# Performance work log

Hardware: AMD Instinct MI355X
Metric: run time of the kernel (lower is better)

The kernel has to match this reference:

```python
import jax, jax.numpy as jnp
import numpy as np

B_, N, C, H = 2048, 49, 384, 12
WH, WW = 7, 7
HEAD_DIM = C // H
SCALE = HEAD_DIM ** -0.5
TABLE = (2 * WH - 1) * (2 * WW - 1)  # 169


def _relative_position_index():
    coords = np.stack(np.meshgrid(np.arange(WH), np.arange(WW), indexing='ij'))  # [2,Wh,Ww]
    flat = coords.reshape(2, -1)  # [2,N]
    rel = flat[:, :, None] - flat[:, None, :]  # [2,N,N]
    rel = rel.transpose(1, 2, 0).astype(np.int32)  # [N,N,2]
    rel[:, :, 0] += WH - 1
    rel[:, :, 1] += WW - 1
    rel[:, :, 0] *= 2 * WW - 1
    return rel.sum(-1)  # [N,N] int32 in [0,169)


def setup_inputs() -> dict:
    key = jax.random.key(0)
    ks = jax.random.split(key, 8)
    return {
        'x': jax.random.normal(ks[0], (B_, N, C), jnp.float32),
        'mask': jax.random.normal(ks[1], (B_, 1, N, N), jnp.float32),
        'stagein': jax.random.uniform(ks[2], (B_, N, C), jnp.float32),
        'rel_bias_table': jax.random.normal(ks[3], (TABLE, H), jnp.float32) * 0.02,
        'rel_pos_index': jnp.asarray(_relative_position_index()),
        'qkv_w': jax.random.normal(ks[4], (3 * C, C), jnp.float32) * 0.02,
        'qkv_b': jax.random.normal(ks[5], (3 * C,), jnp.float32) * 0.02,
        'proj_w': jax.random.normal(ks[6], (C, C), jnp.float32) * 0.02,
        'proj_b': jax.random.normal(ks[7], (C,), jnp.float32) * 0.02,
    }


def reference(x, mask, stagein, rel_bias_table, rel_pos_index, qkv_w, qkv_b, proj_w, proj_b):
    x = x * stagein  # stagein is not None branch
    qkv = x @ qkv_w.T + qkv_b  # [B_, N, 3C]
    qkv = qkv.reshape(B_, N, 3, H, HEAD_DIM).transpose(2, 0, 3, 1, 4)  # [3,B_,H,N,hd]
    q, k, v = qkv[0], qkv[1], qkv[2]
    q = q * SCALE
    attn = jnp.einsum('bhnd,bhmd->bhnm', q, k)  # [B_,H,N,N]
    # relative position bias gather: [N*N] -> [N,N,H] -> [1,H,N,N]
    bias = rel_bias_table[rel_pos_index.reshape(-1)].reshape(N, N, H)
    bias = bias.transpose(2, 0, 1)[None]
    attn = jax.nn.softmax(attn + bias + mask, axis=-1)
    out = jnp.einsum('bhnm,bhmd->bhnd', attn, v)  # [B_,H,N,hd]
    out = out.transpose(0, 2, 1, 3).reshape(B_, N, C)
    return out @ proj_w.T + proj_b
```

## Files before the change

### kernel.cpp

```cpp
#include <hip/hip_runtime.h>
#include <hip/hip_bf16.h>
#include <stdint.h>

#define NWIN 2048
#define NTOK 49
#define CDIM 384
#define NHEAD 12
#define HD 32
#define C3 1152
#define NN2 2401
#define MROWS 100352

typedef __bf16 bf16x8 __attribute__((ext_vector_type(8)));
typedef float f32x4 __attribute__((ext_vector_type(4)));
typedef uint32_t u32x4 __attribute__((ext_vector_type(4)));
typedef unsigned int u32;

static __device__ __forceinline__ unsigned short f2bf(float f) {
  uint32_t u = __builtin_bit_cast(uint32_t, f);
  u += 0x7fffu + ((u >> 16) & 1u);
  return (unsigned short)(u >> 16);
}

static __device__ __forceinline__ u32 pk2(float a, float b) {
  return (u32)f2bf(a) | ((u32)f2bf(b) << 16);
}

static __device__ __forceinline__ void gload_lds16(const void* g, void* l) {
  __builtin_amdgcn_global_load_lds((const __attribute__((address_space(1))) void*)g,
                                   (__attribute__((address_space(3))) void*)l,
                                   16, 0, 0);
}

static __device__ __forceinline__ bf16x8 zero8() {
  u32x4 z = {0u, 0u, 0u, 0u};
  return __builtin_bit_cast(bf16x8, z);
}

__global__ void prep_kernel(const float* __restrict__ qkv_w, const float* __restrict__ proj_w,
                            const float* __restrict__ table, const int* __restrict__ idx,
                            unsigned short* __restrict__ wq, unsigned short* __restrict__ wp,
                            float* __restrict__ biasT) {
  const int NW1 = C3 * CDIM;
  const int NW2 = CDIM * CDIM;
  const int NB = NHEAD * NN2;
  int i = blockIdx.x * blockDim.x + threadIdx.x;
  int stride = gridDim.x * blockDim.x;
  for (int t = i; t < NW1 + NW2 + NB; t += stride) {
    if (t < NW1) {
      wq[t] = f2bf(qkv_w[t]);
    } else if (t < NW1 + NW2) {
      int j = t - NW1;
      wp[j] = f2bf(proj_w[j]);
    } else {
      int j = t - NW1 - NW2;
      int h = j / NN2;
      int nm = j - h * NN2;
      int m = nm / 49, n = nm - m * 49;
      biasT[j] = table[idx[n * 49 + m] * NHEAD + h];
    }
  }
}

__global__ void mul_kernel(const float4* __restrict__ x, const float4* __restrict__ s,
                           u32x4* __restrict__ A, int n8) {
  int i0 = blockIdx.x * blockDim.x + threadIdx.x;
  int stride = gridDim.x * blockDim.x;
  for (int t = i0; t < n8; t += stride) {
    float4 a0 = x[2 * t], a1 = x[2 * t + 1];
    float4 b0 = s[2 * t], b1 = s[2 * t + 1];
    u32x4 o;
    o[0] = pk2(a0.x * b0.x, a0.y * b0.y);
    o[1] = pk2(a0.z * b0.z, a0.w * b0.w);
    o[2] = pk2(a1.x * b1.x, a1.y * b1.y);
    o[3] = pk2(a1.z * b1.z, a1.w * b1.w);
    A[t] = o;
  }
}

__launch_bounds__(512, 2)
__global__ void qkv_gemm(const unsigned short* __restrict__ A,
                         const unsigned short* __restrict__ Bw,
                         const float* __restrict__ qkvb,
                         unsigned short* __restrict__ qo,
                         unsigned short* __restrict__ ko,
                         unsigned short* __restrict__ vo) {
  __shared__ unsigned short As[128 * 64];
  __shared__ unsigned short Bs[128 * 64];
  const int tid = threadIdx.x;
  const int w = tid >> 6, l = tid & 63;
  const int l15 = l & 15, lhi = l >> 4;
  const int wgid = (blockIdx.x & 7) * 882 + (blockIdx.x >> 3);
  const int mt = wgid / 9, nt = wgid - mt * 9;
  const int wr = w >> 2, wc = w & 3;
  const int srow = tid >> 3;
  const int scb = (tid & 7) ^ (srow & 7);
  const unsigned short* Ag = A + (size_t)(mt * 128 + srow) * CDIM + scb * 8;
  const unsigned short* Bg = Bw + (size_t)(nt * 128 + srow) * CDIM + scb * 8;
  unsigned short* Asl = As + srow * 64 + (tid & 7) * 8;
  unsigned short* Bsl = Bs + srow * 64 + (tid & 7) * 8;
  const f32x4 z4 = {0.f, 0.f, 0.f, 0.f};
  f32x4 acc[4][2];
#pragma unroll
  for (int m = 0; m < 4; ++m)
#pragma unroll
    for (int n = 0; n < 2; ++n) acc[m][n] = z4;
  const int xr = l15 & 7;
  for (int kt = 0; kt < 6; ++kt) {
    const unsigned short* ag = Ag + kt * 64;
    const unsigned short* bg = Bg + kt * 64;
    gload_lds16(ag, Asl);
    gload_lds16(ag + 64 * CDIM, Asl + 4096);
    gload_lds16(bg, Bsl);
    gload_lds16(bg + 64 * CDIM, Bsl + 4096);
    __syncthreads();
#pragma unroll
    for (int kk = 0; kk < 2; ++kk) {
      const int sl = ((kk << 2) | lhi) ^ xr;
      bf16x8 af[4], bfr[2];
#pragma unroll
      for (int m = 0; m < 4; ++m)
        af[m] = *(const bf16x8*)(As + (wr * 64 + m * 16 + l15) * 64 + sl * 8);
#pragma unroll
      for (int n = 0; n < 2; ++n)
        bfr[n] = *(const bf16x8*)(Bs + (wc * 32 + n * 16 + l15) * 64 + sl * 8);
#pragma unroll
      for (int m = 0; m < 4; ++m)
#pragma unroll
        for (int n = 0; n < 2; ++n)
          acc[m][n] = __builtin_amdgcn_mfma_f32_16x16x32_bf16(af[m], bfr[n], acc[m][n], 0, 0, 0);
    }
    __syncthreads();
  }
  const float SCALE_F = 0.17677669529663687f;
  const int six = nt * 4 + wc;
  const int which = six / 12;
  const int cbase = (six - which * 12) * 32;
  unsigned short* outw = (which == 0) ? qo : ((which == 1) ? ko : vo);
  const float* bptr = qkvb + which * CDIM;
  float bv2[2];
#pragma unroll
  for (int n = 0; n < 2; ++n) bv2[n] = bptr[cbase + n * 16 + l15];
#pragma unroll
  for (int m = 0; m < 4; ++m) {
    const int r0 = mt * 128 + wr * 64 + m * 16 + lhi * 4;
#pragma unroll
    for (int j = 0; j < 4; ++j) {
      unsigned short* orow = outw + (size_t)(r0 + j) * CDIM;
#pragma unroll
      for (int n = 0; n < 2; ++n) {
        float val = acc[m][n][j] + bv2[n];
        if (which == 0) val *= SCALE_F;
        orow[cbase + n * 16 + l15] = f2bf(val);
      }
    }
  }
}

__launch_bounds__(768, 2)
__global__ void attn_kernel(const unsigned short* __restrict__ q,
                            const unsigned short* __restrict__ kmat,
                            const unsigned short* __restrict__ vmat,
                            const float* __restrict__ mask,
                            const float* __restrict__ biasT,
                            unsigned short* __restrict__ attnout) {
  __shared__ unsigned short vT_lds[12][32 * 72];
  __shared__ float maskLds[49 * 50];
  const int tid = threadIdx.x;
  const int w = tid >> 6, l = tid & 63;
  const int l15 = l & 15, lhi = l >> 4;
  const int b = (blockIdx.x & 7) * 256 + (blockIdx.x >> 3);
  unsigned short* Vw = &vT_lds[w][0];
  const f32x4 z4 = {0.f, 0.f, 0.f, 0.f};
  const int h = w;
  const size_t rowbase = (size_t)b * NTOK * CDIM + h * HD;
  const unsigned short* qb = q + rowbase;
  const unsigned short* kb = kmat + rowbase;
  const unsigned short* vb = vmat + rowbase;
  {
    const float* mb = mask + (size_t)b * NN2;
    for (int i = tid; i < NN2; i += 768) {
      const int n = i / 49, m = i - n * 49;
      maskLds[m * 50 + n] = mb[i];
    }
  }
  {
    const int n = l;
    unsigned short tmp[32];
    if (n < 49) {
      *(u32x4*)(&tmp[0])  = *(const u32x4*)(vb + (size_t)n * CDIM);
      *(u32x4*)(&tmp[8])  = *(const u32x4*)(vb + (size_t)n * CDIM + 8);
      *(u32x4*)(&tmp[16]) = *(const u32x4*)(vb + (size_t)n * CDIM + 16);
      *(u32x4*)(&tmp[24]) = *(const u32x4*)(vb + (size_t)n * CDIM + 24);
    } else {
#pragma unroll
      for (int d2 = 0; d2 < 32; ++d2) tmp[d2] = 0;
    }
#pragma unroll
    for (int d2 = 0; d2 < 32; ++d2) Vw[d2 * 72 + n] = tmp[d2];
  }
  bf16x8 aq[4], bk[4];
#pragma unroll
  for (int t = 0; t < 4; ++t) {
    const int row = t * 16 + l15;
    if (row < 49) {
      aq[t] = *(const bf16x8*)(qb + (size_t)row * CDIM + lhi * 8);
      bk[t] = *(const bf16x8*)(kb + (size_t)row * CDIM + lhi * 8);
    } else {
      aq[t] = zero8();
      bk[t] = zero8();
    }
  }
  __syncthreads();
  const float* biash = biasT + h * NN2;
  u32 P4[4][4][2];
#pragma unroll
  for (int nt = 0; nt < 4; ++nt) {
    f32x4 s4[4];
#pragma unroll
    for (int mt = 0; mt < 4; ++mt)
      s4[mt] = __builtin_amdgcn_mfma_f32_16x16x32_bf16(bk[mt], aq[nt], z4, 0, 0, 0);
    const int n = nt * 16 + l15;
#pragma unroll
    for (int mt = 0; mt < 4; ++mt) {
#pragma unroll
      for (int r = 0; r < 4; ++r) {
        const int m = mt * 16 + lhi * 4 + r;
        float val = -1e30f;
        if (n < 49 && m < 49)
          val = s4[mt][r] + biash[m * 49 + n] + maskLds[m * 50 + n];
        s4[mt][r] = val;
      }
    }
    float mx = s4[0][0];
#pragma unroll
    for (int mt = 0; mt < 4; ++mt)
#pragma unroll
      for (int r = 0; r < 4; ++r) mx = fmaxf(mx, s4[mt][r]);
    mx = fmaxf(mx, __shfl_xor(mx, 16));
    mx = fmaxf(mx, __shfl_xor(mx, 32));
    float sum = 0.f;
#pragma unroll
    for (int mt = 0; mt < 4; ++mt)
#pragma unroll
      for (int r = 0; r < 4; ++r) {
        s4[mt][r] = __expf(s4[mt][r] - mx);
        sum += s4[mt][r];
      }
    sum += __shfl_xor(sum, 16);
    sum += __shfl_xor(sum, 32);
    const float rinv = 1.0f / sum;
#pragma unroll
    for (int mt = 0; mt < 4; ++mt) {
      P4[nt][mt][0] = pk2(s4[mt][0] * rinv, s4[mt][1] * rinv);
      P4[nt][mt][1] = pk2(s4[mt][2] * rinv, s4[mt][3] * rinv);
    }
  }
  const int sA = ((l >> 4) & 1) * 32 + l15;
  const int sB = sA + 16;
  const bool hi_sel = (l & 32) != 0;
  f32x4 o[4][2];
#pragma unroll
  for (int ti = 0; ti < 4; ++ti) { o[ti][0] = z4; o[ti][1] = z4; }
#pragma unroll
  for (int kk = 0; kk < 2; ++kk) {
    bf16x8 bv0 = *(const bf16x8*)(Vw + l15 * 72 + kk * 32 + lhi * 8);
    bf16x8 bv1 = *(const bf16x8*)(Vw + (16 + l15) * 72 + kk * 32 + lhi * 8);
#pragma unroll
    for (int ti = 0; ti < 4; ++ti) {
      int x0 = __shfl((int)P4[ti][2 * kk][0], sA);
      int x1 = __shfl((int)P4[ti][2 * kk][1], sA);
      int y0 = __shfl((int)P4[ti][2 * kk + 1][0], sA);
      int y1 = __shfl((int)P4[ti][2 * kk + 1][1], sA);
      int x2 = __shfl((int)P4[ti][2 * kk][0], sB);
      int x3 = __shfl((int)P4[ti][2 * kk][1], sB);
      int y2 = __shfl((int)P4[ti][2 * kk + 1][0], sB);
      int y3 = __shfl((int)P4[ti][2 * kk + 1][1], sB);
      u32x4 f;
      f[0] = (u32)(hi_sel ? y0 : x0);
      f[1] = (u32)(hi_sel ? y1 : x1);
      f[2] = (u32)(hi_sel ? y2 : x2);
      f[3] = (u32)(hi_sel ? y3 : x3);
      bf16x8 pa = __builtin_bit_cast(bf16x8, f);
      o[ti][0] = __builtin_amdgcn_mfma_f32_16x16x32_bf16(pa, bv0, o[ti][0], 0, 0, 0);
      o[ti][1] = __builtin_amdgcn_mfma_f32_16x16x32_bf16(pa, bv1, o[ti][1], 0, 0, 0);
    }
  }
#pragma unroll
  for (int ti = 0; ti < 4; ++ti) {
#pragma unroll
    for (int r = 0; r < 4; ++r) {
      const int n = ti * 16 + lhi * 4 + r;
      if (n < 49) {
        unsigned short* orow = attnout + ((size_t)b * NTOK + n) * CDIM + h * HD;
        orow[l15] = f2bf(o[ti][0][r]);
        orow[16 + l15] = f2bf(o[ti][1][r]);
      }
    }
  }
}

__launch_bounds__(512, 2)
__global__ void proj_gemm(const unsigned short* __restrict__ A,
                          const unsigned short* __restrict__ Bw,
                          const float* __restrict__ pb,
                          float* __restrict__ out) {
  __shared__ unsigned short As[128 * 64];
  __shared__ unsigned short Bs[128 * 64];
  const int tid = threadIdx.x;
  const int w = tid >> 6, l = tid & 63;
  const int l15 = l & 15, lhi = l >> 4;
  const int wgid = (blockIdx.x & 7) * 294 + (blockIdx.x >> 3);
  const int mt = wgid / 3, nt = wgid - mt * 3;
  const int wr = w >> 2, wc = w & 3;
  const int srow = tid >> 3;
  const int scb = (tid & 7) ^ (srow & 7);
  const unsigned short* Ag = A + (size_t)(mt * 128 + srow) * CDIM + scb * 8;
  const unsigned short* Bg = Bw + (size_t)(nt * 128 + srow) * CDIM + scb * 8;
  unsigned short* Asl = As + srow * 64 + (tid & 7) * 8;
  unsigned short* Bsl = Bs + srow * 64 + (tid & 7) * 8;
  const f32x4 z4 = {0.f, 0.f, 0.f, 0.f};
  f32x4 acc[4][2];
#pragma unroll
  for (int m = 0; m < 4; ++m)
#pragma unroll
    for (int n = 0; n < 2; ++n) acc[m][n] = z4;
  const int xr = l15 & 7;
  for (int kt = 0; kt < 6; ++kt) {
    const unsigned short* ag = Ag + kt * 64;
    const unsigned short* bg = Bg + kt * 64;
    gload_lds16(ag, Asl);
    gload_lds16(ag + 64 * CDIM, Asl + 4096);
    gload_lds16(bg, Bsl);
    gload_lds16(bg + 64 * CDIM, Bsl + 4096);
    __syncthreads();
#pragma unroll
    for (int kk = 0; kk < 2; ++kk) {
      const int sl = ((kk << 2) | lhi) ^ xr;
      bf16x8 af[4], bfr[2];
#pragma unroll
      for (int m = 0; m < 4; ++m)
        af[m] = *(const bf16x8*)(As + (wr * 64 + m * 16 + l15) * 64 + sl * 8);
#pragma unroll
      for (int n = 0; n < 2; ++n)
        bfr[n] = *(const bf16x8*)(Bs + (wc * 32 + n * 16 + l15) * 64 + sl * 8);
#pragma unroll
      for (int m = 0; m < 4; ++m)
#pragma unroll
        for (int n = 0; n < 2; ++n)
          acc[m][n] = __builtin_amdgcn_mfma_f32_16x16x32_bf16(af[m], bfr[n], acc[m][n], 0, 0, 0);
    }
    __syncthreads();
  }
#pragma unroll
  for (int m = 0; m < 4; ++m) {
    const int r0 = mt * 128 + wr * 64 + m * 16 + lhi * 4;
#pragma unroll
    for (int j = 0; j < 4; ++j) {
      float* orow = out + (size_t)(r0 + j) * CDIM;
#pragma unroll
      for (int n = 0; n < 2; ++n) {
        const int c = nt * 128 + wc * 32 + n * 16 + l15;
        orow[c] = acc[m][n][j] + pb[c];
      }
    }
  }
}

extern "C" void kernel_launch(void* const* d_in, const int* in_sizes, int n_in,
                              void* d_out, int out_size, void* d_ws, size_t ws_size,
                              hipStream_t stream) {
  const float* x       = (const float*)d_in[0];
  const float* mask    = (const float*)d_in[1];
  const float* stagein = (const float*)d_in[2];
  const float* table   = (const float*)d_in[3];
  const int*   idx     = (const int*)d_in[4];
  const float* qkv_w   = (const float*)d_in[5];
  const float* qkv_b   = (const float*)d_in[6];
  const float* proj_w  = (const float*)d_in[7];
  const float* proj_b  = (const float*)d_in[8];
  float* out = (float*)d_out;
  char* ws = (char*)d_ws;

  const size_t SZA = (size_t)MROWS * CDIM * 2;
  unsigned short* Abf = (unsigned short*)(ws);
  unsigned short* qb  = (unsigned short*)(ws + SZA);
  unsigned short* kb  = (unsigned short*)(ws + 2 * SZA);
  unsigned short* vb  = (unsigned short*)(ws + 3 * SZA);
  unsigned short* wq  = (unsigned short*)(ws + 4 * SZA);
  unsigned short* wp  = (unsigned short*)(ws + 4 * SZA + (size_t)C3 * CDIM * 2);
  float* biasT        = (float*)(ws + 4 * SZA + (size_t)C3 * CDIM * 2 + (size_t)CDIM * CDIM * 2);
  unsigned short* attnout = Abf;

  prep_kernel<<<dim3(512), dim3(256), 0, stream>>>(qkv_w, proj_w, table, idx, wq, wp, biasT);
  mul_kernel<<<dim3(2048), dim3(256), 0, stream>>>((const float4*)x, (const float4*)stagein,
                                                   (u32x4*)Abf, MROWS * CDIM / 8);
  qkv_gemm<<<dim3(784 * 9), dim3(512), 0, stream>>>(Abf, wq, qkv_b, qb, kb, vb);
  attn_kernel<<<dim3(NWIN), dim3(768), 0, stream>>>(qb, kb, vb, mask, biasT, attnout);
  proj_gemm<<<dim3(784 * 3), dim3(512), 0, stream>>>(attnout, wp, proj_b, out);
}
```

Measured before the change: 407.2 us.

## Fuse output projection GEMM into attention kernel via LDS-staged per-window output

Drops the separate proj_gemm kernel. Each attention workgroup now writes its per-window output (49x384 bf16) into swizzled LDS, reusing the V-transpose buffer, then each wave computes a 32-column slice of the projection with MFMA, reading weight fragments directly from global memory. This removes the bf16 attention-output round trip through HBM and one kernel launch. In exchange, each workgroup re-reads the full projection weight from global memory or L2, and an extra barrier is added.

```diff
diff --git a/kernel.cpp b/kernel.cpp
--- a/kernel.cpp
+++ b/kernel.cpp
@@ -163,14 +163,18 @@
                             const unsigned short* __restrict__ vmat,
                             const float* __restrict__ mask,
                             const float* __restrict__ biasT,
-                            unsigned short* __restrict__ attnout) {
-  __shared__ unsigned short vT_lds[12][32 * 72];
+                            const unsigned short* __restrict__ wp,
+                            const float* __restrict__ pb,
+                            float* __restrict__ out) {
+  __shared__ __align__(16) char shraw[12 * 32 * 72 * 2];
   __shared__ float maskLds[49 * 50];
+  unsigned short* vT = (unsigned short*)shraw;
+  unsigned short* Ost = (unsigned short*)shraw;
   const int tid = threadIdx.x;
   const int w = tid >> 6, l = tid & 63;
   const int l15 = l & 15, lhi = l >> 4;
   const int b = (blockIdx.x & 7) * 256 + (blockIdx.x >> 3);
-  unsigned short* Vw = &vT_lds[w][0];
+  unsigned short* Vw = vT + w * (32 * 72);
   const f32x4 z4 = {0.f, 0.f, 0.f, 0.f};
   const int h = w;
   const size_t rowbase = (size_t)b * NTOK * CDIM + h * HD;
@@ -286,82 +290,61 @@
       o[ti][1] = __builtin_amdgcn_mfma_f32_16x16x32_bf16(pa, bv1, o[ti][1], 0, 0, 0);
     }
   }
+  __syncthreads();
 #pragma unroll
   for (int ti = 0; ti < 4; ++ti) {
 #pragma unroll
     for (int r = 0; r < 4; ++r) {
       const int n = ti * 16 + lhi * 4 + r;
       if (n < 49) {
-        unsigned short* orow = attnout + ((size_t)b * NTOK + n) * CDIM + h * HD;
-        orow[l15] = f2bf(o[ti][0][r]);
-        orow[16 + l15] = f2bf(o[ti][1][r]);
-      }
-    }
-  }
-}
-
-__launch_bounds__(512, 2)
-__global__ void proj_gemm(const unsigned short* __restrict__ A,
-                          const unsigned short* __restrict__ Bw,
-                          const float* __restrict__ pb,
-                          float* __restrict__ out) {
-  __shared__ unsigned short As[128 * 64];
-  __shared__ unsigned short Bs[128 * 64];
-  const int tid = threadIdx.x;
-  const int w = tid >> 6, l = tid & 63;
-  const int l15 = l & 15, lhi = l >> 4;
-  const int wgid = (blockIdx.x & 7) * 294 + (blockIdx.x >> 3);
-  const int mt = wgid / 3, nt = wgid - mt * 3;
-  const int wr = w >> 2, wc = w & 3;
-  const int srow = tid >> 3;
-  const int scb = (tid & 7) ^ (srow & 7);
-  const unsigned short* Ag = A + (size_t)(mt * 128 + srow) * CDIM + scb * 8;
-  const unsigned short* Bg = Bw + (size_t)(nt * 128 + srow) * CDIM + scb * 8;
-  unsigned short* Asl = As + srow * 64 + (tid & 7) * 8;
-  unsigned short* Bsl = Bs + srow * 64 + (tid & 7) * 8;
-  const f32x4 z4 = {0.f, 0.f, 0.f, 0.f};
-  f32x4 acc[4][2];
-#pragma unroll
-  for (int m = 0; m < 4; ++m)
-#pragma unroll
-    for (int n = 0; n < 2; ++n) acc[m][n] = z4;
-  const int xr = l15 & 7;
-  for (int kt = 0; kt < 6; ++kt) {
-    const unsigned short* ag = Ag + kt * 64;
-    const unsigned short* bg = Bg + kt * 64;
-    gload_lds16(ag, Asl);
-    gload_lds16(ag + 64 * CDIM, Asl + 4096);
-    gload_lds16(bg, Bsl);
-    gload_lds16(bg + 64 * CDIM, Bsl + 4096);
-    __syncthreads();
-#pragma unroll
-    for (int kk = 0; kk < 2; ++kk) {
-      const int sl = ((kk << 2) | lhi) ^ xr;
-      bf16x8 af[4], bfr[2];
-#pragma unroll
-      for (int m = 0; m < 4; ++m)
-        af[m] = *(const bf16x8*)(As + (wr * 64 + m * 16 + l15) * 64 + sl * 8);
-#pragma unroll
-      for (int n = 0; n < 2; ++n)
-        bfr[n] = *(const bf16x8*)(Bs + (wc * 32 + n * 16 + l15) * 64 + sl * 8);
-#pragma unroll
-      for (int m = 0; m < 4; ++m)
-#pragma unroll
-        for (int n = 0; n < 2; ++n)
-          acc[m][n] = __builtin_amdgcn_mfma_f32_16x16x32_bf16(af[m], bfr[n], acc[m][n], 0, 0, 0);
-    }
-    __syncthreads();
-  }
+#pragma unroll
+        for (int half = 0; half < 2; ++half) {
+          const int c = h * HD + half * 16 + l15;
+          const int cb = (c >> 3) ^ (n & 7);
+          Ost[n * CDIM + cb * 8 + (c & 7)] = f2bf(o[ti][half][r]);
+        }
+      }
+    }
+  }
+  {
+    const int i = tid;
+    if (i < 15 * 48) {
+      const int row = 49 + i / 48, cb = i - (i / 48) * 48;
+      const u32x4 z = {0u, 0u, 0u, 0u};
+      *(u32x4*)(Ost + row * CDIM + cb * 8) = z;
+    }
+  }
+  __syncthreads();
+  f32x4 acc2[4][2];
+#pragma unroll
+  for (int m = 0; m < 4; ++m) { acc2[m][0] = z4; acc2[m][1] = z4; }
+  const int xk = l15 & 7;
+#pragma unroll
+  for (int ks = 0; ks < 12; ++ks) {
+    bf16x8 af[4], bw2[2];
+#pragma unroll
+    for (int m = 0; m < 4; ++m)
+      af[m] = *(const bf16x8*)(Ost + (m * 16 + l15) * CDIM + (((ks * 4 + lhi) ^ xk) * 8));
+#pragma unroll
+    for (int n2 = 0; n2 < 2; ++n2)
+      bw2[n2] = *(const bf16x8*)(wp + (size_t)(h * HD + n2 * 16 + l15) * CDIM + ks * 32 + lhi * 8);
+#pragma unroll
+    for (int m = 0; m < 4; ++m)
+#pragma unroll
+      for (int n2 = 0; n2 < 2; ++n2)
+        acc2[m][n2] = __builtin_amdgcn_mfma_f32_16x16x32_bf16(af[m], bw2[n2], acc2[m][n2], 0, 0, 0);
+  }
+  const float pb0 = pb[h * HD + l15];
+  const float pb1 = pb[h * HD + 16 + l15];
 #pragma unroll
   for (int m = 0; m < 4; ++m) {
-    const int r0 = mt * 128 + wr * 64 + m * 16 + lhi * 4;
 #pragma unroll
     for (int j = 0; j < 4; ++j) {
-      float* orow = out + (size_t)(r0 + j) * CDIM;
-#pragma unroll
-      for (int n = 0; n < 2; ++n) {
-        const int c = nt * 128 + wc * 32 + n * 16 + l15;
-        orow[c] = acc[m][n][j] + pb[c];
+      const int n = m * 16 + lhi * 4 + j;
+      if (n < 49) {
+        float* orow = out + ((size_t)b * NTOK + n) * CDIM + h * HD;
+        orow[l15] = acc2[m][0][j] + pb0;
+        orow[16 + l15] = acc2[m][1][j] + pb1;
       }
     }
   }
@@ -390,12 +373,10 @@
   unsigned short* wq  = (unsigned short*)(ws + 4 * SZA);
   unsigned short* wp  = (unsigned short*)(ws + 4 * SZA + (size_t)C3 * CDIM * 2);
   float* biasT        = (float*)(ws + 4 * SZA + (size_t)C3 * CDIM * 2 + (size_t)CDIM * CDIM * 2);
-  unsigned short* attnout = Abf;
 
   prep_kernel<<<dim3(512), dim3(256), 0, stream>>>(qkv_w, proj_w, table, idx, wq, wp, biasT);
   mul_kernel<<<dim3(2048), dim3(256), 0, stream>>>((const float4*)x, (const float4*)stagein,
                                                    (u32x4*)Abf, MROWS * CDIM / 8);
   qkv_gemm<<<dim3(784 * 9), dim3(512), 0, stream>>>(Abf, wq, qkv_b, qb, kb, vb);
-  attn_kernel<<<dim3(NWIN), dim3(768), 0, stream>>>(qb, kb, vb, mask, biasT, attnout);
-  proj_gemm<<<dim3(784 * 3), dim3(512), 0, stream>>>(attnout, wp, proj_b, out);
-}
+  attn_kernel<<<dim3(NWIN), dim3(768), 0, stream>>>(qb, kb, vb, mask, biasT, wp, proj_b, out);
+}
```

New measurement: 450.1 us. 10.5% more time.
